# Performance work log

Hardware: AMD Instinct MI355X
Metric: run time of the kernel (lower is better)

The kernel has to match this reference:

```python
import jax, jax.numpy as jnp
import numpy as np

DIM = 768
NUM_HEADS = 12
HEAD_DIM = DIM // NUM_HEADS
SCALE = HEAD_DIM ** -0.5


def setup_inputs() -> dict:
    key = jax.random.key(0)
    k_x, k_qkv, k_pw, k_pb = jax.random.split(key, 4)
    x = jax.random.normal(k_x, (1, 4096, DIM), dtype=jnp.float32)
    # nn.Linear weights stored as [out, in]; apply as x @ W.T
    w_qkv = jax.random.normal(k_qkv, (3 * DIM, DIM), dtype=jnp.float32) * (DIM ** -0.5)
    w_proj = jax.random.normal(k_pw, (DIM, DIM), dtype=jnp.float32) * (DIM ** -0.5)
    b_proj = jax.random.normal(k_pb, (DIM,), dtype=jnp.float32) * 0.01
    return {"x": x, "w_qkv": w_qkv, "w_proj": w_proj, "b_proj": b_proj}


def reference(x, w_qkv, w_proj, b_proj):
    b, s, d = x.shape
    qkv = jnp.einsum('bsd,ed->bse', x, w_qkv)            # [B,S,3D]
    qkv = qkv.reshape(b, s, 3, NUM_HEADS, HEAD_DIM)
    qkv = jnp.transpose(qkv, (2, 0, 3, 1, 4))            # [3,B,H,S,hd]
    q, k, v = qkv[0], qkv[1], qkv[2]
    scores = jnp.einsum('bhqe,bhke->bhqk', q, k) * SCALE  # [B,H,S,S]
    probs = jax.nn.softmax(scores, axis=-1)
    attended = jnp.einsum('bhqk,bhke->bhqe', probs, v)    # [B,H,S,hd]
    attended = jnp.transpose(attended, (0, 2, 1, 3)).reshape(b, s, d)
    return jnp.einsum('bsd,ed->bse', attended, w_proj) + b_proj
```

## Files before the change

kernel.cpp:

```cpp
#include <hip/hip_runtime.h>
#include <hip/hip_bf16.h>

using short8 = __attribute__((ext_vector_type(8))) short;
using s16x4  = __attribute__((ext_vector_type(4))) short;
using f32x4  = __attribute__((ext_vector_type(4))) float;
using f32x16 = __attribute__((ext_vector_type(16))) float;
using v2i    = __attribute__((ext_vector_type(2))) int;

#define DIM   768
#define D3    2304
#define QKS   1536
#define SEQL  4096
#define NHEAD 12
#define NSPLIT 2

#if defined(__has_builtin)
#  if __has_builtin(__builtin_amdgcn_permlane32_swap)
#    define HAVE_PLSWAP 1
#  endif
#endif

static __device__ __forceinline__ short f2bs(float f) {
  union { __hip_bfloat16 h; short s; } u;
  u.h = __float2bfloat16(f);
  return u.s;
}

static __device__ __forceinline__ float bf2f(short s) {
  union { unsigned u; float f; } x;
  x.u = ((unsigned)(unsigned short)s) << 16;
  return x.f;
}

static __device__ __forceinline__ int cvtpk(float lo, float hi) {
  int r;
  asm("v_cvt_pk_bf16_f32 %0, %1, %2" : "=v"(r) : "v"(lo), "v"(hi));
  return r;
}

static __device__ __forceinline__ float ex2(float x) {
  float r;
  asm("v_exp_f32 %0, %1" : "=v"(r) : "v"(x));
  return r;
}

static __device__ __forceinline__ void gl_lds16(const void* g, void* lds) {
  __builtin_amdgcn_global_load_lds((const __attribute__((address_space(1))) void*)g,
                                   (__attribute__((address_space(3))) void*)lds, 16, 0, 0);
}

__global__ __launch_bounds__(256) void cvt3_kernel(const float* __restrict__ x,
                                                   const float* __restrict__ wq,
                                                   const float* __restrict__ wp,
                                                   short* __restrict__ xb,
                                                   short* __restrict__ wqb,
                                                   short* __restrict__ wpb) {
  int b = blockIdx.x;
  const float* src; short* dst; int base; float sc = 1.0f;
  if (b < 3072)      { src = x;  dst = xb;  base = b * 1024; }
  else if (b < 4800) { src = wq; dst = wqb; base = (b - 3072) * 1024;
                       if (base < DIM * DIM) sc = 0.125f * 1.4426950408889634f; }
  else               { src = wp; dst = wpb; base = (b - 4800) * 1024; }
  int i = base + threadIdx.x * 4;
  f32x4 v = *(const f32x4*)(src + i);
  s16x4 o;
  #pragma unroll
  for (int j = 0; j < 4; ++j) o[j] = f2bs(v[j] * sc);
  *(s16x4*)(dst + i) = o;
}

__global__ __launch_bounds__(256) void gemm_qkv(const short* __restrict__ xb,
                                                const short* __restrict__ wqb,
                                                short* __restrict__ qkb,
                                                short* __restrict__ vtg) {
  __shared__ short As[128 * 64];
  __shared__ short Bs[128 * 64];
  const int bx = blockIdx.x, by = blockIdx.y;
  const short *A, *B; short* C; int m0, n0, ldc;
  if (bx < 12) { A = xb;                     B = wqb; C = qkb; m0 = by * 128; n0 = bx * 128;        ldc = QKS; }
  else         { A = wqb + 1536 * DIM;       B = xb;  C = vtg; m0 = (bx - 12) * 128; n0 = by * 128; ldc = SEQL; }

  const int tid = threadIdx.x;
  const int l  = tid & 63;
  const int w  = tid >> 6;
  const int g  = l >> 4, lc = l & 15;
  const int wr = w >> 1, wc = w & 1;
  const int trow = tid >> 3;
  const int tcol = (tid & 7) * 8;
  const int sswz = 8 * (trow & 7);
  const int rswz = 8 * (lc & 7);

  f32x4 acc[4][4];
  #pragma unroll
  for (int a = 0; a < 4; ++a)
    #pragma unroll
    for (int b = 0; b < 4; ++b) acc[a][b] = (f32x4){0.f, 0.f, 0.f, 0.f};

  for (int k0 = 0; k0 < DIM; k0 += 64) {
    __syncthreads();
    #pragma unroll
    for (int i = 0; i < 4; ++i) {
      int row = i * 32 + trow;
      gl_lds16(A + (size_t)(m0 + row) * DIM + k0 + (tcol ^ sswz), As + row * 64 + tcol);
      gl_lds16(B + (size_t)(n0 + row) * DIM + k0 + (tcol ^ sswz), Bs + row * 64 + tcol);
    }
    __syncthreads();
    #pragma unroll
    for (int kk = 0; kk < 2; ++kk) {
      short8 af[4], bf[4];
      #pragma unroll
      for (int mt = 0; mt < 4; ++mt)
        af[mt] = *(const short8*)(As + (wr * 64 + mt * 16 + lc) * 64 + ((kk * 32 + g * 8) ^ rswz));
      #pragma unroll
      for (int nt = 0; nt < 4; ++nt)
        bf[nt] = *(const short8*)(Bs + (wc * 64 + nt * 16 + lc) * 64 + ((kk * 32 + g * 8) ^ rswz));
      #pragma unroll
      for (int mt = 0; mt < 4; ++mt)
        #pragma unroll
        for (int nt = 0; nt < 4; ++nt)
          acc[mt][nt] = __builtin_amdgcn_mfma_f32_16x16x32_bf16(af[mt], bf[nt], acc[mt][nt], 0, 0, 0);
    }
  }

  #pragma unroll
  for (int mt = 0; mt < 4; ++mt)
    #pragma unroll
    for (int nt = 0; nt < 4; ++nt)
      #pragma unroll
      for (int r = 0; r < 4; ++r) {
        int row = m0 + wr * 64 + mt * 16 + g * 4 + r;
        int col = n0 + wc * 64 + nt * 16 + lc;
        C[(size_t)row * ldc + col] = f2bs(acc[mt][nt][r]);
      }
}

template <bool BF16OUT>
__global__ __launch_bounds__(256) void gemm_bt64(const short* __restrict__ A,
                                                 const short* __restrict__ B,
                                                 short* __restrict__ Cb,
                                                 float* __restrict__ Cf,
                                                 const float* __restrict__ bias,
                                                 int M, int N, int K) {
  __shared__ short As[64 * 64];
  __shared__ short Bs[64 * 64];
  const int tid = threadIdx.x;
  const int l  = tid & 63;
  const int w  = tid >> 6;
  const int g  = l >> 4, lc = l & 15;
  const int wr = w >> 1, wc = w & 1;
  const int m0 = blockIdx.y * 64, n0 = blockIdx.x * 64;
  const int rswz = 8 * (lc & 7);

  f32x4 acc[2][2];
  #pragma unroll
  for (int a = 0; a < 2; ++a)
    #pragma unroll
    for (int b = 0; b < 2; ++b) acc[a][b] = (f32x4){0.f, 0.f, 0.f, 0.f};

  for (int k0 = 0; k0 < K; k0 += 64) {
    __syncthreads();
    #pragma unroll
    for (int i = 0; i < 2; ++i) {
      int seg = i * 256 + tid;
      int row = seg >> 3, c = (seg & 7) * 8;
      int swz = 8 * (row & 7);
      gl_lds16(A + (size_t)(m0 + row) * K + k0 + (c ^ swz), As + seg * 8);
      gl_lds16(B + (size_t)(n0 + row) * K + k0 + (c ^ swz), Bs + seg * 8);
    }
    __syncthreads();
    #pragma unroll
    for (int kk = 0; kk < 2; ++kk) {
      short8 af[2], bf[2];
      #pragma unroll
      for (int mt = 0; mt < 2; ++mt)
        af[mt] = *(const short8*)(As + (wr * 32 + mt * 16 + lc) * 64 + ((kk * 32 + g * 8) ^ rswz));
      #pragma unroll
      for (int nt = 0; nt < 2; ++nt)
        bf[nt] = *(const short8*)(Bs + (wc * 32 + nt * 16 + lc) * 64 + ((kk * 32 + g * 8) ^ rswz));
      #pragma unroll
      for (int mt = 0; mt < 2; ++mt)
        #pragma unroll
        for (int nt = 0; nt < 2; ++nt)
          acc[mt][nt] = __builtin_amdgcn_mfma_f32_16x16x32_bf16(af[mt], bf[nt], acc[mt][nt], 0, 0, 0);
    }
  }

  #pragma unroll
  for (int mt = 0; mt < 2; ++mt)
    #pragma unroll
    for (int nt = 0; nt < 2; ++nt)
      #pragma unroll
      for (int r = 0; r < 4; ++r) {
        int row = m0 + wr * 32 + mt * 16 + g * 4 + r;
        int col = n0 + wc * 32 + nt * 16 + lc;
        float v = acc[mt][nt][r];
        if (BF16OUT) Cb[(size_t)row * N + col] = f2bs(v);
        else         Cf[(size_t)row * N + col] = v + bias[col];
      }
}

__global__ __launch_bounds__(256) void attn_kernel(const short* __restrict__ qkb,
                                                   const short* __restrict__ vtg,
                                                   short* __restrict__ O0,
                                                   short* __restrict__ O1,
                                                   float* __restrict__ Lp,
                                                   int tpb) {
  __shared__ short Ks[3][64 * 64];
  __shared__ short Vt[3][64 * 64];

  const int lin = blockIdx.x;
  const int swz = (lin & 7) * 96 + (lin >> 3);
  const int qt   = swz & 31;
  const int head = (swz >> 5) % NHEAD;
  const int z    = swz / (32 * NHEAD);

  const int tid = threadIdx.x;
  const int l = tid & 63, w = tid >> 6;
  const int h = l >> 5;
  const int q5 = l & 31;
  const int hoff = head * 64;
  const int qbase = qt * 128 + w * 32;
  const int t0 = z * tpb, tend = t0 + tpb;

  short8 qf[4];
  {
    const short* qrow = qkb + (size_t)(qbase + q5) * QKS + hoff;
    #pragma unroll
    for (int ks = 0; ks < 4; ++ks) qf[ks] = *(const short8*)(qrow + ks * 16 + h * 8);
  }

  f32x16 o[2], o_l;
  #pragma unroll
  for (int nt = 0; nt < 2; ++nt)
    #pragma unroll
    for (int r = 0; r < 16; ++r) o[nt][r] = 0.f;
  #pragma unroll
  for (int r = 0; r < 16; ++r) o_l[r] = 0.f;
  const f32x16 zacc = {};
  const short8 ones8 = {(short)0x3F80, (short)0x3F80, (short)0x3F80, (short)0x3F80,
                        (short)0x3F80, (short)0x3F80, (short)0x3F80, (short)0x3F80};

  const int swzK = 8 * (q5 & 7);

  const int srow = tid >> 3, scol = (tid & 7) * 8;
  const int sswz = 8 * (srow & 7);
  const short* kptr = qkb + (size_t)(t0 * 64 + srow) * QKS + hoff + 768 + (scol ^ sswz);
  const short* vptr = vtg + ((size_t)hoff + srow) * 4096 + t0 * 64 + (scol ^ sswz);

  #define STAGE(BUF)                                                             \
    {                                                                            \
      gl_lds16(kptr,             &Ks[BUF][tid * 8]);                             \
      gl_lds16(kptr + 32 * QKS,  &Ks[BUF][(tid + 256) * 8]);                     \
      gl_lds16(vptr,             &Vt[BUF][tid * 8]);                             \
      gl_lds16(vptr + 32 * 4096, &Vt[BUF][(tid + 256) * 8]);                     \
      kptr += 64 * QKS;                                                          \
      vptr += 64;                                                                \
    }

  STAGE(0);
  STAGE(1);

  int cur = 0, sb = 2;
  for (int tt = t0; tt < tend; ++tt) {
    if (tt + 1 < tend) asm volatile("s_waitcnt vmcnt(4)" ::: "memory");
    else               asm volatile("s_waitcnt vmcnt(0)" ::: "memory");
    __builtin_amdgcn_s_barrier();
    if (tt + 2 < tend) STAGE(sb);

    f32x16 p[2];
    __builtin_amdgcn_s_setprio(1);
    #pragma unroll
    for (int ks = 0; ks < 4; ++ks) {
      #pragma unroll
      for (int mt = 0; mt < 2; ++mt) {
        short8 kf = *(const short8*)(&Ks[cur][(mt * 32 + q5) * 64
                                              + ((ks * 16 + h * 8) ^ swzK)]);
        p[mt] = __builtin_amdgcn_mfma_f32_32x32x16_bf16(kf, qf[ks],
                                                        ks == 0 ? zacc : p[mt], 0, 0, 0);
      }
    }
    __builtin_amdgcn_s_setprio(0);

    #pragma unroll
    for (int mt = 0; mt < 2; ++mt)
      #pragma unroll
      for (int i = 0; i < 16; ++i) p[mt][i] = ex2(p[mt][i]);

    int D[16];
    #pragma unroll
    for (int mt = 0; mt < 2; ++mt)
      #pragma unroll
      for (int c = 0; c < 4; ++c) {
        D[mt * 8 + c * 2 + 0] = cvtpk(p[mt][4 * c + 0], p[mt][4 * c + 1]);
        D[mt * 8 + c * 2 + 1] = cvtpk(p[mt][4 * c + 2], p[mt][4 * c + 3]);
      }

    __builtin_amdgcn_s_setprio(1);
    #pragma unroll
    for (int ks = 0; ks < 4; ++ks) {
      union { int i[4]; short8 s; } pa;
#ifdef HAVE_PLSWAP
      v2i r02 = __builtin_amdgcn_permlane32_swap(D[4 * ks + 0], D[4 * ks + 2], false, false);
      v2i r13 = __builtin_amdgcn_permlane32_swap(D[4 * ks + 1], D[4 * ks + 3], false, false);
      pa.i[0] = r02[0];
      pa.i[1] = r13[0];
      pa.i[2] = r02[1];
      pa.i[3] = r13[1];
#else
      const bool hh = (h != 0);
      const int a0 = D[4 * ks + 0], a1 = D[4 * ks + 1];
      const int b0 = D[4 * ks + 2], b1 = D[4 * ks + 3];
      int snd0 = hh ? a0 : b0, snd1 = hh ? a1 : b1;
      int r0 = __shfl_xor(snd0, 32), r1 = __shfl_xor(snd1, 32);
      pa.i[0] = hh ? r0 : a0;
      pa.i[1] = hh ? r1 : a1;
      pa.i[2] = hh ? b0 : r0;
      pa.i[3] = hh ? b1 : r1;
#endif
      o_l = __builtin_amdgcn_mfma_f32_32x32x16_bf16(pa.s, ones8, o_l, 0, 0, 0);
      #pragma unroll
      for (int nt = 0; nt < 2; ++nt) {
        short8 vf = *(const short8*)(&Vt[cur][(nt * 32 + q5) * 64
                                              + ((ks * 16 + h * 8) ^ swzK)]);
        o[nt] = __builtin_amdgcn_mfma_f32_32x32x16_bf16(pa.s, vf, o[nt], 0, 0, 0);
      }
    }
    __builtin_amdgcn_s_setprio(0);

    cur = (cur == 2) ? 0 : cur + 1;
    sb  = (sb == 2) ? 0 : sb + 1;
  }

  if (q5 == 0) {
    #pragma unroll
    for (int pp = 0; pp < 4; ++pp)
      #pragma unroll
      for (int r = 0; r < 4; ++r)
        Lp[(size_t)z * SEQL * NHEAD + (qbase + r + 8 * pp + 4 * h) * NHEAD + head] = o_l[4 * pp + r];
  }
  short* Ob = (z == 0) ? O0 : O1;
  #pragma unroll
  for (int nt = 0; nt < 2; ++nt)
    #pragma unroll
    for (int pp = 0; pp < 4; ++pp)
      #pragma unroll
      for (int r = 0; r < 4; ++r) {
        int q = qbase + r + 8 * pp + 4 * h;
        int d = hoff + nt * 32 + q5;
        Ob[(size_t)q * DIM + d] = f2bs(o[nt][4 * pp + r]);
      }
}

__global__ __launch_bounds__(256) void combine_kernel(short* __restrict__ O0,
                                                      const short* __restrict__ O1,
                                                      const float* __restrict__ Lp) {
  int idx = blockIdx.x * 256 + threadIdx.x;
  int e0 = idx * 8;
  if (e0 >= SEQL * DIM) return;
  int q = e0 / DIM, col = e0 % DIM, head = col >> 6;
  float lv = Lp[q * NHEAD + head] + Lp[SEQL * NHEAD + q * NHEAD + head];
  float inv = 1.0f / lv;
  short8 a = *(const short8*)(O0 + e0);
  short8 b = *(const short8*)(O1 + e0);
  short8 r;
  #pragma unroll
  for (int j = 0; j < 8; ++j) r[j] = f2bs((bf2f(a[j]) + bf2f(b[j])) * inv);
  *(short8*)(O0 + e0) = r;
}

extern "C" void kernel_launch(void* const* d_in, const int* in_sizes, int n_in,
                              void* d_out, int out_size, void* d_ws, size_t ws_size,
                              hipStream_t stream) {
  (void)in_sizes; (void)n_in; (void)out_size; (void)ws_size;
  const float* x      = (const float*)d_in[0];
  const float* w_qkv  = (const float*)d_in[1];
  const float* w_proj = (const float*)d_in[2];
  const float* b_proj = (const float*)d_in[3];
  float* out = (float*)d_out;

  short* xb   = (short*)d_ws;
  short* wqb  = xb  + (size_t)SEQL * DIM;
  short* wpb  = wqb + (size_t)D3 * DIM;
  short* qkb  = wpb + (size_t)DIM * DIM;
  short* attb = qkb + (size_t)SEQL * QKS;
  short* Opart1 = xb;
  float* Lpart  = (float*)wqb;
  short* vtg    = (short*)d_out;

  cvt3_kernel<<<5376, 256, 0, stream>>>(x, w_qkv, w_proj, xb, wqb, wpb);
  gemm_qkv<<<dim3(18, 32), 256, 0, stream>>>(xb, wqb, qkb, vtg);
  attn_kernel<<<dim3(32 * NHEAD * NSPLIT, 1, 1), 256, 0, stream>>>(qkb, vtg, attb, Opart1, Lpart,
                                                                   (SEQL / 64) / NSPLIT);
  combine_kernel<<<SEQL * DIM / 8 / 256, 256, 0, stream>>>(attb, Opart1, Lpart);
  gemm_bt64<false><<<dim3(DIM / 64, SEQL / 64), 256, 0, stream>>>(attb, wpb, nullptr, out, b_proj, SEQL, DIM, DIM);
}
```

Before: 130.0 us.

## Split attention KV range three ways and use double-buffered LDS staging

Attention now splits the key range across three partitions instead of two, launching more blocks, each handling about 21 key tiles. A third partial-output buffer is placed in the unused half of the output buffer, and the combine kernel sums three partials and three row-sum terms. K/V staging drops from a three-deep to a two-deep LDS ring with a full vmcnt(0) wait each iteration, which cuts LDS per block and may allow more resident blocks. In exchange, load/compute overlap shrinks, and the combine step does extra memory traffic for the third partial.

```diff
diff --git a/kernel.cpp b/kernel.cpp
--- a/kernel.cpp
+++ b/kernel.cpp
@@ -12,7 +12,7 @@
 #define QKS   1536
 #define SEQL  4096
 #define NHEAD 12
-#define NSPLIT 2
+#define NSPLIT 3
 
 #if defined(__has_builtin)
 #  if __has_builtin(__builtin_amdgcn_permlane32_swap)
@@ -77,8 +77,8 @@
   __shared__ short Bs[128 * 64];
   const int bx = blockIdx.x, by = blockIdx.y;
   const short *A, *B; short* C; int m0, n0, ldc;
-  if (bx < 12) { A = xb;                     B = wqb; C = qkb; m0 = by * 128; n0 = bx * 128;        ldc = QKS; }
-  else         { A = wqb + 1536 * DIM;       B = xb;  C = vtg; m0 = (bx - 12) * 128; n0 = by * 128; ldc = SEQL; }
+  if (bx < 12) { A = xb;               B = wqb; C = qkb; m0 = by * 128; n0 = bx * 128;        ldc = QKS; }
+  else         { A = wqb + 1536 * DIM; B = xb;  C = vtg; m0 = (bx - 12) * 128; n0 = by * 128; ldc = SEQL; }
 
   const int tid = threadIdx.x;
   const int l  = tid & 63;
@@ -203,13 +203,13 @@
                                                    const short* __restrict__ vtg,
                                                    short* __restrict__ O0,
                                                    short* __restrict__ O1,
-                                                   float* __restrict__ Lp,
-                                                   int tpb) {
-  __shared__ short Ks[3][64 * 64];
-  __shared__ short Vt[3][64 * 64];
+                                                   short* __restrict__ O2,
+                                                   float* __restrict__ Lp) {
+  __shared__ short Ks[2][64 * 64];
+  __shared__ short Vt[2][64 * 64];
 
   const int lin = blockIdx.x;
-  const int swz = (lin & 7) * 96 + (lin >> 3);
+  const int swz = (lin & 7) * 144 + (lin >> 3);
   const int qt   = swz & 31;
   const int head = (swz >> 5) % NHEAD;
   const int z    = swz / (32 * NHEAD);
@@ -220,7 +220,7 @@
   const int q5 = l & 31;
   const int hoff = head * 64;
   const int qbase = qt * 128 + w * 32;
-  const int t0 = z * tpb, tend = t0 + tpb;
+  const int t0 = (z * 64) / 3, tend = ((z + 1) * 64) / 3;
 
   short8 qf[4];
   {
@@ -258,14 +258,12 @@
     }
 
   STAGE(0);
-  STAGE(1);
-
-  int cur = 0, sb = 2;
+
   for (int tt = t0; tt < tend; ++tt) {
-    if (tt + 1 < tend) asm volatile("s_waitcnt vmcnt(4)" ::: "memory");
-    else               asm volatile("s_waitcnt vmcnt(0)" ::: "memory");
+    const int cur = (tt - t0) & 1;
+    asm volatile("s_waitcnt vmcnt(0)" ::: "memory");
     __builtin_amdgcn_s_barrier();
-    if (tt + 2 < tend) STAGE(sb);
+    if (tt + 1 < tend) STAGE(cur ^ 1);
 
     f32x16 p[2];
     __builtin_amdgcn_s_setprio(1);
@@ -326,9 +324,6 @@
       }
     }
     __builtin_amdgcn_s_setprio(0);
-
-    cur = (cur == 2) ? 0 : cur + 1;
-    sb  = (sb == 2) ? 0 : sb + 1;
   }
 
   if (q5 == 0) {
@@ -338,7 +333,7 @@
       for (int r = 0; r < 4; ++r)
         Lp[(size_t)z * SEQL * NHEAD + (qbase + r + 8 * pp + 4 * h) * NHEAD + head] = o_l[4 * pp + r];
   }
-  short* Ob = (z == 0) ? O0 : O1;
+  short* Ob = (z == 0) ? O0 : (z == 1) ? O1 : O2;
   #pragma unroll
   for (int nt = 0; nt < 2; ++nt)
     #pragma unroll
@@ -353,18 +348,22 @@
 
 __global__ __launch_bounds__(256) void combine_kernel(short* __restrict__ O0,
                                                       const short* __restrict__ O1,
+                                                      const short* __restrict__ O2,
                                                       const float* __restrict__ Lp) {
   int idx = blockIdx.x * 256 + threadIdx.x;
   int e0 = idx * 8;
   if (e0 >= SEQL * DIM) return;
   int q = e0 / DIM, col = e0 % DIM, head = col >> 6;
-  float lv = Lp[q * NHEAD + head] + Lp[SEQL * NHEAD + q * NHEAD + head];
+  int i0 = q * NHEAD + head;
+  float lv = Lp[i0] + Lp[SEQL * NHEAD + i0] + Lp[2 * SEQL * NHEAD + i0];
   float inv = 1.0f / lv;
   short8 a = *(const short8*)(O0 + e0);
   short8 b = *(const short8*)(O1 + e0);
+  short8 c = *(const short8*)(O2 + e0);
   short8 r;
   #pragma unroll
-  for (int j = 0; j < 8; ++j) r[j] = f2bs((bf2f(a[j]) + bf2f(b[j])) * inv);
+  for (int j = 0; j < 8; ++j)
+    r[j] = f2bs((bf2f(a[j]) + bf2f(b[j]) + bf2f(c[j])) * inv);
   *(short8*)(O0 + e0) = r;
 }
 
@@ -386,11 +385,11 @@
   short* Opart1 = xb;
   float* Lpart  = (float*)wqb;
   short* vtg    = (short*)d_out;
+  short* Opart2 = vtg + (size_t)SEQL * DIM;
 
   cvt3_kernel<<<5376, 256, 0, stream>>>(x, w_qkv, w_proj, xb, wqb, wpb);
   gemm_qkv<<<dim3(18, 32), 256, 0, stream>>>(xb, wqb, qkb, vtg);
-  attn_kernel<<<dim3(32 * NHEAD * NSPLIT, 1, 1), 256, 0, stream>>>(qkb, vtg, attb, Opart1, Lpart,
-                                                                   (SEQL / 64) / NSPLIT);
-  combine_kernel<<<SEQL * DIM / 8 / 256, 256, 0, stream>>>(attb, Opart1, Lpart);
+  attn_kernel<<<dim3(32 * NHEAD * NSPLIT, 1, 1), 256, 0, stream>>>(qkb, vtg, attb, Opart1, Opart2, Lpart);
+  combine_kernel<<<SEQL * DIM / 8 / 256, 256, 0, stream>>>(attb, Opart1, Opart2, Lpart);
   gemm_bt64<false><<<dim3(DIM / 64, SEQL / 64), 256, 0, stream>>>(attb, wpb, nullptr, out, b_proj, SEQL, DIM, DIM);
 }
```

Result: slower. 135.9 us (+4.5%).
